# Performance work log

Measured on AMD Instinct MI355X. Metric: run time of the kernel, lower is better.

Reference implementation:

```python
import jax, jax.numpy as jnp
import numpy as np

D_MODEL, D_K, H = 1024, 64, 16
B, S = 2, 2048

def setup_inputs() -> dict:
    key = jax.random.key(0)
    ks = jax.random.split(key, 9)
    s_in = 1.0 / np.sqrt(D_MODEL)
    x = jax.random.normal(ks[0], (B, S, D_MODEL), dtype=jnp.float32)
    Wq = jax.random.uniform(ks[1], (H, D_MODEL, D_K), jnp.float32, -s_in, s_in)
    bq = jax.random.uniform(ks[2], (H, D_K), jnp.float32, -s_in, s_in)
    Wk = jax.random.uniform(ks[3], (H, D_MODEL, D_K), jnp.float32, -s_in, s_in)
    bk = jax.random.uniform(ks[4], (H, D_K), jnp.float32, -s_in, s_in)
    Wv = jax.random.uniform(ks[5], (H, D_MODEL, D_K), jnp.float32, -s_in, s_in)
    bv = jax.random.uniform(ks[6], (H, D_K), jnp.float32, -s_in, s_in)
    Wo = jax.random.uniform(ks[7], (D_MODEL, D_MODEL), jnp.float32, -s_in, s_in)
    bo = jax.random.uniform(ks[8], (D_MODEL,), jnp.float32, -s_in, s_in)
    return {"x": x, "Wq": Wq, "bq": bq, "Wk": Wk, "bk": bk,
            "Wv": Wv, "bv": bv, "Wo": Wo, "bo": bo}

def reference(x, Wq, bq, Wk, bk, Wv, bv, Wo, bo):
    # PositionLinear = Linear + ReLU (the ReLU is part of the original math)
    Q = jax.nn.relu(jnp.einsum('bsd,hdk->bhsk', x, Wq) + bq[:, None, :])
    K = jax.nn.relu(jnp.einsum('bsd,hdk->bhsk', x, Wk) + bk[:, None, :])
    V = jax.nn.relu(jnp.einsum('bsd,hdk->bhsk', x, Wv) + bv[:, None, :])
    scale = jnp.sqrt(jnp.float32(Q.shape[-1]))
    scores = jnp.einsum('bhsk,bhtk->bhst', Q, K) / scale  # [B,H,S,S]
    attn = jax.nn.softmax(scores, axis=-1)
    ctx = jnp.einsum('bhst,bhtk->bhsk', attn, V)
    # concat heads along feature dim (head order matches torch.cat(output, 2))
    ctx = jnp.transpose(ctx, (0, 2, 1, 3)).reshape(x.shape[0], x.shape[1], -1)
    out = jax.nn.relu(ctx @ Wo + bo)
    return out
```

## Files before the change

### kernel.cpp

```cpp
#include <hip/hip_runtime.h>
#include <cstddef>

#define D_MODEL 1024
#define DK 64
#define NH 16
#define NB 2
#define SEQ 2048

typedef __attribute__((ext_vector_type(8))) short bf16x8;
typedef __attribute__((ext_vector_type(4))) float floatx4;
typedef __attribute__((ext_vector_type(2))) unsigned uintx2;

static __device__ __forceinline__ unsigned short f2bf(float f) {
    union { float f; unsigned u; } v; v.f = f;
    unsigned r = (v.u + 0x7fffu + ((v.u >> 16) & 1u)) >> 16;
    return (unsigned short)r;
}

static __device__ __forceinline__ unsigned pk2bf(float lo, float hi) {
    unsigned ua = __float_as_uint(lo) + 0x8000u;
    unsigned ub = __float_as_uint(hi) + 0x8000u;
    return __builtin_amdgcn_perm(ub, ua, 0x07060302u);
}

static __device__ __forceinline__ void gld16(const unsigned short* g, unsigned short* l) {
    __builtin_amdgcn_global_load_lds(
        (const __attribute__((address_space(1))) unsigned int*)g,
        (__attribute__((address_space(3))) unsigned int*)l, 16, 0, 0);
}

__global__ __launch_bounds__(256) void prep(
    const float* __restrict__ x, unsigned short* __restrict__ xb,
    const float* __restrict__ Wq, const float* __restrict__ Wk,
    const float* __restrict__ Wv, const float* __restrict__ Wo,
    unsigned short* __restrict__ Bqkv, unsigned short* __restrict__ Bo)
{
    __shared__ float T[64][65];
    const int tid = threadIdx.x;

    if (blockIdx.x < 1024) {
        const size_t i = ((size_t)blockIdx.x * 256 + tid) * 16;
#pragma unroll
        for (int c = 0; c < 16; c += 4) {
            float4 v = *(const float4*)&x[i + c];
            uint2 pk;
            pk.x = (unsigned)f2bf(v.x) | ((unsigned)f2bf(v.y) << 16);
            pk.y = (unsigned)f2bf(v.z) | ((unsigned)f2bf(v.w) << 16);
            *(uint2*)&xb[i + c] = pk;
        }
        return;
    }

    const int t   = blockIdx.x - 1024;
    const int rr   = tid >> 2;
    const int cseg = (tid & 3) * 16;

    const float* src;
    unsigned short* dst;
    if (t < 768) {
        const int proj = t / 256, rem = t % 256;
        const int h = rem >> 4, d0 = (rem & 15) * 64;
        const float* W = proj == 0 ? Wq : (proj == 1 ? Wk : Wv);
        src = W + ((size_t)h * 1024 + d0) * 64;
#pragma unroll
        for (int c = 0; c < 16; c += 4) {
            float4 v = *(const float4*)&src[(size_t)rr * 64 + cseg + c];
            T[rr][cseg + c + 0] = v.x; T[rr][cseg + c + 1] = v.y;
            T[rr][cseg + c + 2] = v.z; T[rr][cseg + c + 3] = v.w;
        }
        __syncthreads();
        dst = &Bqkv[((size_t)proj * 1024 + h * 64 + rr) * 1024 + d0 + cseg];
    } else {
        const int t2 = t - 768;
        const int k0 = (t2 >> 4) * 64, nb0 = (t2 & 15) * 64;
#pragma unroll
        for (int c = 0; c < 16; c += 4) {
            float4 v = *(const float4*)&Wo[(size_t)(k0 + rr) * 1024 + nb0 + cseg + c];
            T[rr][cseg + c + 0] = v.x; T[rr][cseg + c + 1] = v.y;
            T[rr][cseg + c + 2] = v.z; T[rr][cseg + c + 3] = v.w;
        }
        __syncthreads();
        dst = &Bo[(size_t)(nb0 + rr) * 1024 + k0 + cseg];
    }
    unsigned int w[8];
#pragma unroll
    for (int ii = 0; ii < 8; ii++) {
        unsigned short lo = f2bf(T[cseg + ii * 2 + 0][rr]);
        unsigned short hi = f2bf(T[cseg + ii * 2 + 1][rr]);
        w[ii] = (unsigned)lo | ((unsigned)hi << 16);
    }
    *(uint4*)(dst + 0) = make_uint4(w[0], w[1], w[2], w[3]);
    *(uint4*)(dst + 8) = make_uint4(w[4], w[5], w[6], w[7]);
}

__global__ __launch_bounds__(256) void gemm_qkv(
    const unsigned short* __restrict__ Abf,
    const unsigned short* __restrict__ Bp,
    const float* __restrict__ bq, const float* __restrict__ bk,
    const float* __restrict__ bv,
    unsigned short* __restrict__ Qo, unsigned short* __restrict__ Ko,
    unsigned short* __restrict__ Vo)
{
    __shared__ __align__(16) unsigned short As[128 * 32];
    __shared__ __align__(16) unsigned short Bs[128 * 32];

    const int tid  = threadIdx.x;
    const int wv   = tid >> 6, lane = tid & 63;
    const int m0   = blockIdx.x * 128;
    const int n0   = blockIdx.y * 128;
    const int lq   = lane & 15, g = lane >> 4;
    const int wm   = (wv >> 1) * 64;
    const int wn   = (wv & 1) * 64;
    const int srow = lane >> 2;
    const int sseg = (lane & 3) * 8;

    floatx4 acc[4][4];
#pragma unroll
    for (int i = 0; i < 4; i++)
#pragma unroll
        for (int j = 0; j < 4; j++) acc[i][j] = (floatx4){0.f, 0.f, 0.f, 0.f};

    for (int k0 = 0; k0 < 1024; k0 += 32) {
#pragma unroll
        for (int r = 0; r < 2; r++) {
            const int chunk = wv * 2 + r;
            const int row   = chunk * 16 + srow;
            gld16(&Abf[(size_t)(m0 + row) * 1024 + k0 + sseg], &As[chunk * 512]);
            gld16(&Bp [(size_t)(n0 + row) * 1024 + k0 + sseg], &Bs[chunk * 512]);
        }
        __syncthreads();
        bf16x8 af[4], bfv[4];
#pragma unroll
        for (int i = 0; i < 4; i++)
            af[i] = *(const bf16x8*)&As[(wm + i * 16 + lq) * 32 + g * 8];
#pragma unroll
        for (int j = 0; j < 4; j++)
            bfv[j] = *(const bf16x8*)&Bs[(wn + j * 16 + lq) * 32 + g * 8];
#pragma unroll
        for (int i = 0; i < 4; i++)
#pragma unroll
            for (int j = 0; j < 4; j++)
                acc[i][j] = __builtin_amdgcn_mfma_f32_16x16x32_bf16(af[i], bfv[j], acc[i][j], 0, 0, 0);
        __syncthreads();
    }

    const int proj = n0 >> 10;
    const float* bias = proj == 0 ? bq : (proj == 1 ? bk : bv);
    unsigned short* OutQK = proj == 0 ? Qo : Ko;

#pragma unroll
    for (int j = 0; j < 4; j++) {
        const int n  = n0 + wn + j * 16 + lq;
        const int nn = n & 1023;
        const int h  = nn >> 6, dk = nn & 63;
        const float bb = bias[nn];
#pragma unroll
        for (int i = 0; i < 4; i++) {
            const int mbase = m0 + wm + i * 16 + g * 4;
            const int b_ = mbase >> 11;
            const int s_ = mbase & (SEQ - 1);
            const int bh = b_ * NH + h;
            if (proj < 2) {
                const size_t fb = (((size_t)bh * 128 + (s_ >> 4)) * 2 + (dk >> 5)) * 512
                                + (size_t)((((dk & 31) >> 3) * 16) + (s_ & 15)) * 8 + (dk & 7);
#pragma unroll
                for (int r = 0; r < 4; r++)
                    OutQK[fb + (size_t)r * 8] = f2bf(fmaxf(acc[i][j][r] + bb, 0.f));
            } else {
                const size_t fb = ((((size_t)bh * 32 + (s_ >> 6)) * 4 + (dk >> 4)) * 2
                                   + ((s_ >> 5) & 1)) * 512
                                + (size_t)((((s_ & 31) >> 3) * 16) + (dk & 15)) * 8 + (s_ & 7);
                uint2 pk;
                pk.x = (unsigned)f2bf(fmaxf(acc[i][j][0] + bb, 0.f))
                     | ((unsigned)f2bf(fmaxf(acc[i][j][1] + bb, 0.f)) << 16);
                pk.y = (unsigned)f2bf(fmaxf(acc[i][j][2] + bb, 0.f))
                     | ((unsigned)f2bf(fmaxf(acc[i][j][3] + bb, 0.f)) << 16);
                *(uint2*)&Vo[fb] = pk;
            }
        }
    }
}

__global__ __launch_bounds__(512, 4) void attn_kernel(
    const unsigned short* __restrict__ Qf,
    const unsigned short* __restrict__ Kf,
    const unsigned short* __restrict__ Vf,
    unsigned short* __restrict__ ctxb)
{
    __shared__ __align__(16) unsigned short KVs[2][16384];
    __shared__ float Lx[4][2][64];

    const int blk = blockIdx.x;
    const int xcd = blk & 7;
    const int j_  = blk >> 3;
    const int bh  = xcd * 4 + (j_ & 3);
    const int qt  = j_ >> 2;

    const int tid  = threadIdx.x;
    const int wv   = tid >> 6;
    const int lane = tid & 63;
    const int lq   = lane & 15;
    const int g    = lane >> 4;
    const int qq   = wv >> 1;
    const int kh   = wv & 1;

    const int q0 = qt * 128 + qq * 32;

    bf16x8 qa[2], qb[2];
    const size_t qfB = ((size_t)bh * 128 + (q0 >> 4)) * 1024 + (size_t)lane * 8;
#pragma unroll
    for (int t = 0; t < 2; t++) {
        qa[t] = *(const bf16x8*)&Qf[qfB + (size_t)t * 1024];
        qb[t] = *(const bf16x8*)&Qf[qfB + (size_t)t * 1024 + 512];
    }

    const float C  = 0.18033688011112042f;
    const float MC = 2.8853900817779267f;

    const short one_bf = (short)0x3F80;
    const bf16x8 ones8 = (bf16x8){one_bf, one_bf, one_bf, one_bf,
                                  one_bf, one_bf, one_bf, one_bf};

    const unsigned short* KtB = &Kf[(size_t)bh * 131072];
    const unsigned short* VtB = &Vf[(size_t)bh * 131072];

    floatx4 accl[2];
    floatx4 acc[2][4];
#pragma unroll
    for (int t = 0; t < 2; t++) {
        accl[t] = (floatx4){0.f, 0.f, 0.f, 0.f};
#pragma unroll
        for (int n = 0; n < 4; n++) acc[t][n] = (floatx4){0.f, 0.f, 0.f, 0.f};
    }

#pragma unroll
    for (int r = 0; r < 2; r++) {
        const int c = wv * 2 + r;
        gld16(&KtB[(size_t)c * 512 + lane * 8], &KVs[0][c * 512]);
        gld16(&VtB[(size_t)c * 512 + lane * 8], &KVs[0][8192 + c * 512]);
    }
    __syncthreads();

    for (int jt = 0; jt < SEQ / 128; jt++) {
        const int buf = jt & 1;

        const int jn = (jt + 1) & (SEQ / 128 - 1);
        const unsigned short* ktn = &KtB[(size_t)jn * 8192];
        const unsigned short* vtn = &VtB[(size_t)jn * 8192];
#pragma unroll
        for (int r = 0; r < 2; r++) {
            const int c = wv * 2 + r;
            gld16(&ktn[(size_t)c * 512 + lane * 8], &KVs[buf ^ 1][c * 512]);
            gld16(&vtn[(size_t)c * 512 + lane * 8], &KVs[buf ^ 1][8192 + c * 512]);
        }

        const unsigned short* kb = &KVs[buf][0];
        const unsigned short* vb = &KVs[buf][8192];

#pragma unroll
        for (int s = 0; s < 2; s++) {
            const int kg = 4 * kh + 2 * s;
            bf16x8 a0 = *(const bf16x8*)&kb[(kg + 0) * 1024 + lane * 8];
            bf16x8 a1 = *(const bf16x8*)&kb[(kg + 0) * 1024 + 512 + lane * 8];
            bf16x8 a2 = *(const bf16x8*)&kb[(kg + 1) * 1024 + lane * 8];
            bf16x8 a3 = *(const bf16x8*)&kb[(kg + 1) * 1024 + 512 + lane * 8];
            bf16x8 vr[4];
#pragma unroll
            for (int n = 0; n < 4; n++)
                vr[n] = *(const bf16x8*)&vb[(kh * 4 + n) * 1024 + s * 512 + lane * 8];

#pragma unroll
            for (int t = 0; t < 2; t++) {
                floatx4 s0 = (floatx4){0.f, 0.f, 0.f, 0.f};
                floatx4 s1 = (floatx4){0.f, 0.f, 0.f, 0.f};
                s0 = __builtin_amdgcn_mfma_f32_16x16x32_bf16(a0, qa[t], s0, 0, 0, 0);
                s0 = __builtin_amdgcn_mfma_f32_16x16x32_bf16(a1, qb[t], s0, 0, 0, 0);
                s1 = __builtin_amdgcn_mfma_f32_16x16x32_bf16(a2, qa[t], s1, 0, 0, 0);
                s1 = __builtin_amdgcn_mfma_f32_16x16x32_bf16(a3, qb[t], s1, 0, 0, 0);

                float p00 = __builtin_amdgcn_exp2f(fmaf(s0[0], C, -MC));
                float p01 = __builtin_amdgcn_exp2f(fmaf(s0[1], C, -MC));
                float p02 = __builtin_amdgcn_exp2f(fmaf(s0[2], C, -MC));
                float p03 = __builtin_amdgcn_exp2f(fmaf(s0[3], C, -MC));
                unsigned d0 = pk2bf(p00, p01);
                unsigned d1 = pk2bf(p02, p03);

                float p10 = __builtin_amdgcn_exp2f(fmaf(s1[0], C, -MC));
                float p11 = __builtin_amdgcn_exp2f(fmaf(s1[1], C, -MC));
                float p12 = __builtin_amdgcn_exp2f(fmaf(s1[2], C, -MC));
                float p13 = __builtin_amdgcn_exp2f(fmaf(s1[3], C, -MC));
                unsigned d2 = pk2bf(p10, p11);
                unsigned d3 = pk2bf(p12, p13);

                uintx2 r02 = __builtin_amdgcn_permlane32_swap(d0, d2, false, false);
                uintx2 r13 = __builtin_amdgcn_permlane32_swap(d1, d3, false, false);
                uintx2 f02 = __builtin_amdgcn_permlane16_swap(r02.x, r02.y, false, false);
                uintx2 f13 = __builtin_amdgcn_permlane16_swap(r13.x, r13.y, false, false);

                union { unsigned u[4]; bf16x8 v; } pbu;
                pbu.u[0] = f02.x;
                pbu.u[1] = f13.x;
                pbu.u[2] = f02.y;
                pbu.u[3] = f13.y;

                accl[t] = __builtin_amdgcn_mfma_f32_16x16x32_bf16(ones8, pbu.v, accl[t], 0, 0, 0);

#pragma unroll
                for (int n = 0; n < 4; n++)
                    acc[t][n] = __builtin_amdgcn_mfma_f32_16x16x32_bf16(vr[n], pbu.v, acc[t][n], 0, 0, 0);
            }
        }

        __syncthreads();
    }

    float* red = (float*)&KVs[0][0] + (size_t)qq * 2048;
    if (kh == 1) {
#pragma unroll
        for (int t = 0; t < 2; t++) {
            Lx[qq][t][lane] = accl[t][0];
#pragma unroll
            for (int n = 0; n < 4; n++)
                *(floatx4*)&red[(t * 4 + n) * 256 + lane * 4] = acc[t][n];
        }
    }
    __syncthreads();
    if (kh == 0) {
        const int b_ = bh >> 4, h_ = bh & 15;
#pragma unroll
        for (int t = 0; t < 2; t++) {
            const float lt = accl[t][0] + Lx[qq][t][lane];
            const float li = 1.f / lt;
#pragma unroll
            for (int n = 0; n < 4; n++) {
                floatx4 a = acc[t][n];
                floatx4 b = *(const floatx4*)&red[(t * 4 + n) * 256 + lane * 4];
                uint2 pk;
                pk.x = pk2bf((a[0] + b[0]) * li, (a[1] + b[1]) * li);
                pk.y = pk2bf((a[2] + b[2]) * li, (a[3] + b[3]) * li);
                *(uint2*)&ctxb[((size_t)(b_ * SEQ) + q0 + t * 16 + lq) * D_MODEL
                               + h_ * DK + n * 16 + g * 4] = pk;
            }
        }
    }
}

__global__ __launch_bounds__(256) void gemm_o(
    const unsigned short* __restrict__ Abf,
    const unsigned short* __restrict__ Bp,
    const float* __restrict__ bo,
    float* __restrict__ out)
{
    __shared__ __align__(16) unsigned short As[64 * 32];
    __shared__ __align__(16) unsigned short Bs[64 * 32];

    const int tid  = threadIdx.x;
    const int wv   = tid >> 6, lane = tid & 63;
    const int bid  = blockIdx.x;
    const int swz  = (bid & 7) * 128 + (bid >> 3);
    const int m0   = (swz & 63) * 64;
    const int n0   = (swz >> 6) * 64;
    const int lq   = lane & 15, g = lane >> 4;
    const int wm   = (wv >> 1) * 32;
    const int wn   = (wv & 1) * 32;
    const int srow = lane >> 2;
    const int sseg = (lane & 3) * 8;

    floatx4 acc[2][2];
#pragma unroll
    for (int i = 0; i < 2; i++)
#pragma unroll
        for (int j = 0; j < 2; j++) acc[i][j] = (floatx4){0.f, 0.f, 0.f, 0.f};

    for (int k0 = 0; k0 < 1024; k0 += 32) {
        const int row = wv * 16 + srow;
        gld16(&Abf[(size_t)(m0 + row) * 1024 + k0 + sseg], &As[wv * 512]);
        gld16(&Bp [(size_t)(n0 + row) * 1024 + k0 + sseg], &Bs[wv * 512]);
        __syncthreads();
        bf16x8 af[2], bfv[2];
#pragma unroll
        for (int i = 0; i < 2; i++)
            af[i] = *(const bf16x8*)&As[(wm + i * 16 + lq) * 32 + g * 8];
#pragma unroll
        for (int j = 0; j < 2; j++)
            bfv[j] = *(const bf16x8*)&Bs[(wn + j * 16 + lq) * 32 + g * 8];
#pragma unroll
        for (int i = 0; i < 2; i++)
#pragma unroll
            for (int j = 0; j < 2; j++)
                acc[i][j] = __builtin_amdgcn_mfma_f32_16x16x32_bf16(af[i], bfv[j], acc[i][j], 0, 0, 0);
        __syncthreads();
    }

#pragma unroll
    for (int j = 0; j < 2; j++) {
        const int n  = n0 + wn + j * 16 + lq;
        const float bb = bo[n];
#pragma unroll
        for (int i = 0; i < 2; i++) {
#pragma unroll
            for (int r = 0; r < 4; r++) {
                const int m = m0 + wm + i * 16 + g * 4 + r;
                out[(size_t)m * 1024 + n] = fmaxf(acc[i][j][r] + bb, 0.f);
            }
        }
    }
}

extern "C" void kernel_launch(void* const* d_in, const int* in_sizes, int n_in,
                              void* d_out, int out_size, void* d_ws, size_t ws_size,
                              hipStream_t stream) {
    const float* x  = (const float*)d_in[0];
    const float* Wq = (const float*)d_in[1];
    const float* bq = (const float*)d_in[2];
    const float* Wk = (const float*)d_in[3];
    const float* bk = (const float*)d_in[4];
    const float* Wv = (const float*)d_in[5];
    const float* bv = (const float*)d_in[6];
    const float* Wo = (const float*)d_in[7];
    const float* bo = (const float*)d_in[8];
    float* out = (float*)d_out;

    const size_t perE = (size_t)NB * NH * SEQ * DK;
    unsigned short* xbf  = (unsigned short*)d_ws;
    unsigned short* Bqkv = xbf  + (size_t)4096 * 1024;
    unsigned short* Bo   = Bqkv + (size_t)3072 * 1024;
    unsigned short* Qfr  = Bo   + (size_t)1024 * 1024;
    unsigned short* Kfr  = Qfr + perE;
    unsigned short* Vfr  = Kfr + perE;
    unsigned short* Cbf  = Vfr + perE;

    prep<<<2048, 256, 0, stream>>>(x, xbf, Wq, Wk, Wv, Wo, Bqkv, Bo);
    gemm_qkv<<<dim3(32, 24), 256, 0, stream>>>(xbf, Bqkv, bq, bk, bv, Qfr, Kfr, Vfr);
    attn_kernel<<<512, 512, 0, stream>>>(Qfr, Kfr, Vfr, Cbf);
    gemm_o<<<1024, 256, 0, stream>>>(Cbf, Bo, bo, out);
}
```

Baseline: 184.5 us.

## Halve attention tile sizes to double block count and occupancy

Shrinks the attention kernel's query tile from 128 to 64 rows and its key/value tile from 128 to 64 per iteration, and doubles the grid to 1024 blocks. Shared memory per block drops by half and launch bounds now request 8 blocks per CU, so more waves can be resident to hide latency. In exchange each K/V tile loaded is reused by half as many query rows, which doubles K/V traffic, and the loop runs twice as many iterations with a barrier in each.

```diff
diff --git a/kernel.cpp b/kernel.cpp
--- a/kernel.cpp
+++ b/kernel.cpp
@@ -181,14 +181,14 @@
     }
 }
 
-__global__ __launch_bounds__(512, 4) void attn_kernel(
+__global__ __launch_bounds__(512, 8) void attn_kernel(
     const unsigned short* __restrict__ Qf,
     const unsigned short* __restrict__ Kf,
     const unsigned short* __restrict__ Vf,
     unsigned short* __restrict__ ctxb)
 {
-    __shared__ __align__(16) unsigned short KVs[2][16384];
-    __shared__ float Lx[4][2][64];
+    __shared__ __align__(16) unsigned short KVs[2][8192];
+    __shared__ float Lx[4][64];
 
     const int blk = blockIdx.x;
     const int xcd = blk & 7;
@@ -204,15 +204,11 @@
     const int qq   = wv >> 1;
     const int kh   = wv & 1;
 
-    const int q0 = qt * 128 + qq * 32;
-
-    bf16x8 qa[2], qb[2];
+    const int q0 = qt * 64 + qq * 16;
+
     const size_t qfB = ((size_t)bh * 128 + (q0 >> 4)) * 1024 + (size_t)lane * 8;
-#pragma unroll
-    for (int t = 0; t < 2; t++) {
-        qa[t] = *(const bf16x8*)&Qf[qfB + (size_t)t * 1024];
-        qb[t] = *(const bf16x8*)&Qf[qfB + (size_t)t * 1024 + 512];
-    }
+    bf16x8 qa = *(const bf16x8*)&Qf[qfB];
+    bf16x8 qb = *(const bf16x8*)&Qf[qfB + 512];
 
     const float C  = 0.18033688011112042f;
     const float MC = 2.8853900817779267f;
@@ -224,123 +220,96 @@
     const unsigned short* KtB = &Kf[(size_t)bh * 131072];
     const unsigned short* VtB = &Vf[(size_t)bh * 131072];
 
-    floatx4 accl[2];
-    floatx4 acc[2][4];
-#pragma unroll
-    for (int t = 0; t < 2; t++) {
-        accl[t] = (floatx4){0.f, 0.f, 0.f, 0.f};
-#pragma unroll
-        for (int n = 0; n < 4; n++) acc[t][n] = (floatx4){0.f, 0.f, 0.f, 0.f};
-    }
-
-#pragma unroll
-    for (int r = 0; r < 2; r++) {
-        const int c = wv * 2 + r;
-        gld16(&KtB[(size_t)c * 512 + lane * 8], &KVs[0][c * 512]);
-        gld16(&VtB[(size_t)c * 512 + lane * 8], &KVs[0][8192 + c * 512]);
-    }
+    floatx4 accl = (floatx4){0.f, 0.f, 0.f, 0.f};
+    floatx4 acc[4];
+#pragma unroll
+    for (int n = 0; n < 4; n++) acc[n] = (floatx4){0.f, 0.f, 0.f, 0.f};
+
+    gld16(&KtB[(size_t)wv * 512 + lane * 8], &KVs[0][wv * 512]);
+    gld16(&VtB[(size_t)wv * 512 + lane * 8], &KVs[0][4096 + wv * 512]);
     __syncthreads();
 
-    for (int jt = 0; jt < SEQ / 128; jt++) {
+    for (int jt = 0; jt < SEQ / 64; jt++) {
         const int buf = jt & 1;
 
-        const int jn = (jt + 1) & (SEQ / 128 - 1);
-        const unsigned short* ktn = &KtB[(size_t)jn * 8192];
-        const unsigned short* vtn = &VtB[(size_t)jn * 8192];
-#pragma unroll
-        for (int r = 0; r < 2; r++) {
-            const int c = wv * 2 + r;
-            gld16(&ktn[(size_t)c * 512 + lane * 8], &KVs[buf ^ 1][c * 512]);
-            gld16(&vtn[(size_t)c * 512 + lane * 8], &KVs[buf ^ 1][8192 + c * 512]);
-        }
+        const int jn = (jt + 1) & (SEQ / 64 - 1);
+        gld16(&KtB[(size_t)jn * 4096 + wv * 512 + lane * 8], &KVs[buf ^ 1][wv * 512]);
+        gld16(&VtB[(size_t)jn * 4096 + wv * 512 + lane * 8], &KVs[buf ^ 1][4096 + wv * 512]);
 
         const unsigned short* kb = &KVs[buf][0];
-        const unsigned short* vb = &KVs[buf][8192];
-
-#pragma unroll
-        for (int s = 0; s < 2; s++) {
-            const int kg = 4 * kh + 2 * s;
-            bf16x8 a0 = *(const bf16x8*)&kb[(kg + 0) * 1024 + lane * 8];
-            bf16x8 a1 = *(const bf16x8*)&kb[(kg + 0) * 1024 + 512 + lane * 8];
-            bf16x8 a2 = *(const bf16x8*)&kb[(kg + 1) * 1024 + lane * 8];
-            bf16x8 a3 = *(const bf16x8*)&kb[(kg + 1) * 1024 + 512 + lane * 8];
-            bf16x8 vr[4];
-#pragma unroll
-            for (int n = 0; n < 4; n++)
-                vr[n] = *(const bf16x8*)&vb[(kh * 4 + n) * 1024 + s * 512 + lane * 8];
-
-#pragma unroll
-            for (int t = 0; t < 2; t++) {
-                floatx4 s0 = (floatx4){0.f, 0.f, 0.f, 0.f};
-                floatx4 s1 = (floatx4){0.f, 0.f, 0.f, 0.f};
-                s0 = __builtin_amdgcn_mfma_f32_16x16x32_bf16(a0, qa[t], s0, 0, 0, 0);
-                s0 = __builtin_amdgcn_mfma_f32_16x16x32_bf16(a1, qb[t], s0, 0, 0, 0);
-                s1 = __builtin_amdgcn_mfma_f32_16x16x32_bf16(a2, qa[t], s1, 0, 0, 0);
-                s1 = __builtin_amdgcn_mfma_f32_16x16x32_bf16(a3, qb[t], s1, 0, 0, 0);
-
-                float p00 = __builtin_amdgcn_exp2f(fmaf(s0[0], C, -MC));
-                float p01 = __builtin_amdgcn_exp2f(fmaf(s0[1], C, -MC));
-                float p02 = __builtin_amdgcn_exp2f(fmaf(s0[2], C, -MC));
-                float p03 = __builtin_amdgcn_exp2f(fmaf(s0[3], C, -MC));
-                unsigned d0 = pk2bf(p00, p01);
-                unsigned d1 = pk2bf(p02, p03);
-
-                float p10 = __builtin_amdgcn_exp2f(fmaf(s1[0], C, -MC));
-                float p11 = __builtin_amdgcn_exp2f(fmaf(s1[1], C, -MC));
-                float p12 = __builtin_amdgcn_exp2f(fmaf(s1[2], C, -MC));
-                float p13 = __builtin_amdgcn_exp2f(fmaf(s1[3], C, -MC));
-                unsigned d2 = pk2bf(p10, p11);
-                unsigned d3 = pk2bf(p12, p13);
-
-                uintx2 r02 = __builtin_amdgcn_permlane32_swap(d0, d2, false, false);
-                uintx2 r13 = __builtin_amdgcn_permlane32_swap(d1, d3, false, false);
-                uintx2 f02 = __builtin_amdgcn_permlane16_swap(r02.x, r02.y, false, false);
-                uintx2 f13 = __builtin_amdgcn_permlane16_swap(r13.x, r13.y, false, false);
-
-                union { unsigned u[4]; bf16x8 v; } pbu;
-                pbu.u[0] = f02.x;
-                pbu.u[1] = f13.x;
-                pbu.u[2] = f02.y;
-                pbu.u[3] = f13.y;
-
-                accl[t] = __builtin_amdgcn_mfma_f32_16x16x32_bf16(ones8, pbu.v, accl[t], 0, 0, 0);
-
-#pragma unroll
-                for (int n = 0; n < 4; n++)
-                    acc[t][n] = __builtin_amdgcn_mfma_f32_16x16x32_bf16(vr[n], pbu.v, acc[t][n], 0, 0, 0);
-            }
-        }
-
-        __syncthreads();
-    }
-
-    float* red = (float*)&KVs[0][0] + (size_t)qq * 2048;
+        const unsigned short* vb = &KVs[buf][4096];
+
+        bf16x8 a0 = *(const bf16x8*)&kb[(2 * kh + 0) * 1024 + lane * 8];
+        bf16x8 a1 = *(const bf16x8*)&kb[(2 * kh + 0) * 1024 + 512 + lane * 8];
+        bf16x8 a2 = *(const bf16x8*)&kb[(2 * kh + 1) * 1024 + lane * 8];
+        bf16x8 a3 = *(const bf16x8*)&kb[(2 * kh + 1) * 1024 + 512 + lane * 8];
+        bf16x8 vr[4];
+#pragma unroll
+        for (int n = 0; n < 4; n++)
+            vr[n] = *(const bf16x8*)&vb[(n * 2 + kh) * 512 + lane * 8];
+
+        floatx4 s0 = (floatx4){0.f, 0.f, 0.f, 0.f};
+        floatx4 s1 = (floatx4){0.f, 0.f, 0.f, 0.f};
+        s0 = __builtin_amdgcn_mfma_f32_16x16x32_bf16(a0, qa, s0, 0, 0, 0);
+        s0 = __builtin_amdgcn_mfma_f32_16x16x32_bf16(a1, qb, s0, 0, 0, 0);
+        s1 = __builtin_amdgcn_mfma_f32_16x16x32_bf16(a2, qa, s1, 0, 0, 0);
+        s1 = __builtin_amdgcn_mfma_f32_16x16x32_bf16(a3, qb, s1, 0, 0, 0);
+
+        float p00 = __builtin_amdgcn_exp2f(fmaf(s0[0], C, -MC));
+        float p01 = __builtin_amdgcn_exp2f(fmaf(s0[1], C, -MC));
+        float p02 = __builtin_amdgcn_exp2f(fmaf(s0[2], C, -MC));
+        float p03 = __builtin_amdgcn_exp2f(fmaf(s0[3], C, -MC));
+        unsigned d0 = pk2bf(p00, p01);
+        unsigned d1 = pk2bf(p02, p03);
+
+        float p10 = __builtin_amdgcn_exp2f(fmaf(s1[0], C, -MC));
+        float p11 = __builtin_amdgcn_exp2f(fmaf(s1[1], C, -MC));
+        float p12 = __builtin_amdgcn_exp2f(fmaf(s1[2], C, -MC));
+        float p13 = __builtin_amdgcn_exp2f(fmaf(s1[3], C, -MC));
+        unsigned d2 = pk2bf(p10, p11);
+        unsigned d3 = pk2bf(p12, p13);
+
+        uintx2 r02 = __builtin_amdgcn_permlane32_swap(d0, d2, false, false);
+        uintx2 r13 = __builtin_amdgcn_permlane32_swap(d1, d3, false, false);
+        uintx2 f02 = __builtin_amdgcn_permlane16_swap(r02.x, r02.y, false, false);
+        uintx2 f13 = __builtin_amdgcn_permlane16_swap(r13.x, r13.y, false, false);
+
+        union { unsigned u[4]; bf16x8 v; } pbu;
+        pbu.u[0] = f02.x;
+        pbu.u[1] = f13.x;
+        pbu.u[2] = f02.y;
+        pbu.u[3] = f13.y;
+
+        accl = __builtin_amdgcn_mfma_f32_16x16x32_bf16(ones8, pbu.v, accl, 0, 0, 0);
+
+#pragma unroll
+        for (int n = 0; n < 4; n++)
+            acc[n] = __builtin_amdgcn_mfma_f32_16x16x32_bf16(vr[n], pbu.v, acc[n], 0, 0, 0);
+
+        __syncthreads();
+    }
+
+    float* red = (float*)&KVs[0][0] + (size_t)qq * 1024;
     if (kh == 1) {
-#pragma unroll
-        for (int t = 0; t < 2; t++) {
-            Lx[qq][t][lane] = accl[t][0];
-#pragma unroll
-            for (int n = 0; n < 4; n++)
-                *(floatx4*)&red[(t * 4 + n) * 256 + lane * 4] = acc[t][n];
-        }
+        Lx[qq][lane] = accl[0];
+#pragma unroll
+        for (int n = 0; n < 4; n++)
+            *(floatx4*)&red[n * 256 + lane * 4] = acc[n];
     }
     __syncthreads();
     if (kh == 0) {
         const int b_ = bh >> 4, h_ = bh & 15;
-#pragma unroll
-        for (int t = 0; t < 2; t++) {
-            const float lt = accl[t][0] + Lx[qq][t][lane];
-            const float li = 1.f / lt;
-#pragma unroll
-            for (int n = 0; n < 4; n++) {
-                floatx4 a = acc[t][n];
-                floatx4 b = *(const floatx4*)&red[(t * 4 + n) * 256 + lane * 4];
-                uint2 pk;
-                pk.x = pk2bf((a[0] + b[0]) * li, (a[1] + b[1]) * li);
-                pk.y = pk2bf((a[2] + b[2]) * li, (a[3] + b[3]) * li);
-                *(uint2*)&ctxb[((size_t)(b_ * SEQ) + q0 + t * 16 + lq) * D_MODEL
-                               + h_ * DK + n * 16 + g * 4] = pk;
-            }
+        const float lt = accl[0] + Lx[qq][lane];
+        const float li = 1.f / lt;
+#pragma unroll
+        for (int n = 0; n < 4; n++) {
+            floatx4 a = acc[n];
+            floatx4 b = *(const floatx4*)&red[n * 256 + lane * 4];
+            uint2 pk;
+            pk.x = pk2bf((a[0] + b[0]) * li, (a[1] + b[1]) * li);
+            pk.y = pk2bf((a[2] + b[2]) * li, (a[3] + b[3]) * li);
+            *(uint2*)&ctxb[((size_t)(b_ * SEQ) + q0 + lq) * D_MODEL
+                           + h_ * DK + n * 16 + g * 4] = pk;
         }
     }
 }
@@ -432,6 +401,6 @@
 
     prep<<<2048, 256, 0, stream>>>(x, xbf, Wq, Wk, Wv, Wo, Bqkv, Bo);
     gemm_qkv<<<dim3(32, 24), 256, 0, stream>>>(xbf, Bqkv, bq, bk, bv, Qfr, Kfr, Vfr);
-    attn_kernel<<<512, 512, 0, stream>>>(Qfr, Kfr, Vfr, Cbf);
+    attn_kernel<<<1024, 512, 0, stream>>>(Qfr, Kfr, Vfr, Cbf);
     gemm_o<<<1024, 256, 0, stream>>>(Cbf, Bo, bo, out);
 }
```

Result: slower. 190.4 us (+3.2%).
